# Kernel tuning notes

Measured on AMD Instinct MI355X. Metric: run time of the kernel, lower is better.

The kernel has to match this reference:

```python
import jax, jax.numpy as jnp
import numpy as np

NEIGH = 0.4  # neighborhood_size from the module


def setup_inputs() -> dict:
    key = jax.random.key(0)
    ks = jax.random.split(key, 14)
    N, E, H, G, M = 1024, 64, 128, 8, 20
    OUT = 6 * M
    f32 = jnp.float32
    inp = {
        "xabs": jax.random.uniform(ks[0], (N, 2), f32),
        "i_h0": jax.random.normal(ks[1], (1, N, H), f32) * 0.1,
        "i_c0": jax.random.normal(ks[2], (1, N, H), f32) * 0.1,
        # I_Embedding: Linear(2, E)
        "W_emb": jax.random.normal(ks[3], (E, 2), f32) * 0.5,
        "b_emb": jax.random.normal(ks[4], (E,), f32) * 0.1,
        # embedding_social: Linear(G*G*H, E)
        "W_soc": jax.random.normal(ks[5], (E, G * G * H), f32) * (1.0 / np.sqrt(G * G * H)),
        "b_soc": jax.random.normal(ks[6], (E,), f32) * 0.1,
        # LSTM(2E -> H), torch gate order [i, f, g, o]
        "W_ih": jax.random.normal(ks[7], (4 * H, 2 * E), f32) * (1.0 / np.sqrt(2 * E)),
        "W_hh": jax.random.normal(ks[8], (4 * H, H), f32) * (1.0 / np.sqrt(H)),
        "b_ih": jax.random.normal(ks[9], (4 * H,), f32) * 0.05,
        "b_hh": jax.random.normal(ks[10], (4 * H,), f32) * 0.05,
        # I_Output: Linear(H, 6*M)
        "W_out": jax.random.normal(ks[11], (OUT, H), f32) * (1.0 / np.sqrt(H)),
        "b_out": jax.random.normal(ks[12], (OUT,), f32) * 0.05,
    }
    return inp


def _grid_mask(xabs, G):
    # Vectorized getGridMask: [N, N, G*G] one-hot bin membership.
    N = xabs.shape[0]
    # dx[n, m] = other_x - width_low(n); in-range iff 0 <= dx < NEIGH
    dx = xabs[None, :, 0] - (xabs[:, None, 0] - NEIGH / 2)
    dy = xabs[None, :, 1] - (xabs[:, None, 1] - NEIGH / 2)
    cell_x = jnp.floor(dx / NEIGH * G).astype(jnp.int32)
    cell_y = jnp.floor(dy / NEIGH * G).astype(jnp.int32)
    valid = (dx >= 0) & (dx < NEIGH) & (dy >= 0) & (dy < NEIGH)
    valid &= (cell_x >= 0) & (cell_x < G) & (cell_y >= 0) & (cell_y < G)
    valid &= ~jnp.eye(N, dtype=bool)  # skip self
    cell = jnp.where(valid, cell_x + cell_y * G, 0)
    mask = jax.nn.one_hot(cell, G * G, dtype=xabs.dtype)
    return mask * valid[:, :, None].astype(xabs.dtype)


def reference(xabs, i_h0, i_c0, W_emb, b_emb, W_soc, b_soc,
              W_ih, W_hh, b_ih, b_hh, W_out, b_out):
    N = xabs.shape[0]
    H = i_h0.shape[-1]
    G = int(np.sqrt(W_soc.shape[1] // H))
    M = W_out.shape[0] // 6

    # Input embedding
    emb_x = jax.nn.relu(xabs @ W_emb.T + b_emb)  # [N, E]

    # Social pooling: grid mask + scatter-reduce of hidden states
    h0 = i_h0[0]  # [N, H]
    mask = _grid_mask(xabs, G)  # [N, N, G*G]
    social = jnp.einsum('nmg,md->ngd', mask, h0)  # [N, G*G, H]
    social = social.reshape(N, G * G * H)
    pooling = jax.nn.relu(social @ W_soc.T + b_soc)  # [N, E]

    # Single LSTM step (seq len 1, 1 layer), torch gate order i,f,g,o
    lstm_in = jnp.concatenate([emb_x, pooling], axis=-1)  # [N, 2E]
    gates = lstm_in @ W_ih.T + b_ih + h0 @ W_hh.T + b_hh  # [N, 4H]
    i_g, f_g, g_g, o_g = jnp.split(gates, 4, axis=-1)
    c = jax.nn.sigmoid(f_g) * i_c0[0] + jax.nn.sigmoid(i_g) * jnp.tanh(g_g)
    h = jax.nn.sigmoid(o_g) * jnp.tanh(c)  # [N, H]

    final = h @ W_out.T + b_out  # [N, 6M]
    mu1, mu2, log_sigma1, log_sigma2, rho, pi_logits = jnp.split(final, 6, axis=1)
    return (mu1, mu2, log_sigma1, log_sigma2, rho, pi_logits)
```

## Files before the change

kernel.cpp:

```cpp
#include <hip/hip_runtime.h>
#include <hip/hip_bf16.h>
#include <math.h>

typedef __hip_bfloat16 bf16;
typedef short s8v __attribute__((ext_vector_type(8)));
typedef float f4v __attribute__((ext_vector_type(4)));

__device__ __forceinline__ float b2f(bf16 v) { return __bfloat162float(v); }

template <bool F32>
__device__ __forceinline__ float ld(const void* p, int i) {
  if (F32) return ((const float*)p)[i];
  return b2f(((const bf16*)p)[i]);
}

template <bool F32>
__device__ __forceinline__ s8v ldfrag(const void* p, size_t i) {
  if (F32) {
    const float* f = (const float*)p + i;
    float4 u = *reinterpret_cast<const float4*>(f);
    float4 v = *reinterpret_cast<const float4*>(f + 4);
    s8v r;
    bf16 t;
    t = __float2bfloat16(u.x); r[0] = *(short*)&t;
    t = __float2bfloat16(u.y); r[1] = *(short*)&t;
    t = __float2bfloat16(u.z); r[2] = *(short*)&t;
    t = __float2bfloat16(u.w); r[3] = *(short*)&t;
    t = __float2bfloat16(v.x); r[4] = *(short*)&t;
    t = __float2bfloat16(v.y); r[5] = *(short*)&t;
    t = __float2bfloat16(v.z); r[6] = *(short*)&t;
    t = __float2bfloat16(v.w); r[7] = *(short*)&t;
    return r;
  }
  return *reinterpret_cast<const s8v*>((const bf16*)p + i);
}

__device__ __forceinline__ float sigm(float x) {
  return 0.5f * (1.0f + tanhf(0.5f * x));
}

__device__ __forceinline__ bool detect_f32(const void* xabs) {
  unsigned short v = ((const unsigned short*)xabs)[threadIdx.x & 63];
  int ex = (v >> 7) & 0xFF;
  return __ballot(ex >= 0x93) != 0ull;
}

template <bool F32>
__device__ __forceinline__ void cvt4(const void* src, bf16* __restrict__ dst,
                                     int count, int gt, int gsz) {
  for (int i = gt * 4; i < count; i += gsz * 4) {
    if (F32) {
      float4 v = *reinterpret_cast<const float4*>((const float*)src + i);
      bf16 t[4] = {__float2bfloat16(v.x), __float2bfloat16(v.y),
                   __float2bfloat16(v.z), __float2bfloat16(v.w)};
      *reinterpret_cast<uint2*>(&dst[i]) = *reinterpret_cast<uint2*>(t);
    } else {
      *reinterpret_cast<uint2*>(&dst[i]) =
          *reinterpret_cast<const uint2*>((const bf16*)src + i);
    }
  }
}

template <bool F32>
__device__ __forceinline__ void zgemm_body(const void* h0, const void* Wsoc,
                                           const void* Wih, const void* Whh,
                                           const void* Wout,
                                           bf16* __restrict__ Z, bf16* Wih_b,
                                           bf16* Whh_b, bf16* Wout_b) {
  if (blockIdx.x >= 256) {
    const int gt = (blockIdx.x - 256) * 256 + threadIdx.x;
    const int gsz = 16 * 256;
    cvt4<F32>(Wih, Wih_b, 512 * 128, gt, gsz);
    cvt4<F32>(Whh, Whh_b, 512 * 128, gt, gsz);
    cvt4<F32>(Wout, Wout_b, 120 * 128, gt, gsz);
    return;
  }
  const int wave = threadIdx.x >> 6, lane = threadIdx.x & 63;
  const int mt = blockIdx.x & 15;
  const int g  = (blockIdx.x >> 4) * 4 + wave;
  const int r16 = lane & 15, quad = lane >> 4;

  s8v afr[4][4];
#pragma unroll
  for (int ms = 0; ms < 4; ++ms)
#pragma unroll
    for (int kq = 0; kq < 4; ++kq)
      afr[ms][kq] = ldfrag<F32>(
          h0, (size_t)(mt * 64 + ms * 16 + r16) * 128 + kq * 32 + quad * 8);

  f4v acc[4][4];
#pragma unroll
  for (int ms = 0; ms < 4; ++ms)
#pragma unroll
    for (int t = 0; t < 4; ++t) acc[ms][t] = (f4v){0.f, 0.f, 0.f, 0.f};

#pragma unroll
  for (int t = 0; t < 4; ++t) {
#pragma unroll
    for (int kq = 0; kq < 4; ++kq) {
      s8v bfr = ldfrag<F32>(
          Wsoc, (size_t)(t * 16 + r16) * 8192 + g * 128 + kq * 32 + quad * 8);
#pragma unroll
      for (int ms = 0; ms < 4; ++ms)
        acc[ms][t] = __builtin_amdgcn_mfma_f32_16x16x32_bf16(afr[ms][kq], bfr,
                                                             acc[ms][t], 0, 0, 0);
    }
  }
#pragma unroll
  for (int ms = 0; ms < 4; ++ms)
#pragma unroll
    for (int t = 0; t < 4; ++t)
#pragma unroll
      for (int reg = 0; reg < 4; ++reg)
        Z[(size_t)(mt * 64 + ms * 16 + quad * 4 + reg) * 4096 + g * 64 +
          t * 16 + r16] = __float2bfloat16(acc[ms][t][reg]);
}

__global__ __launch_bounds__(256, 1) void k_zgemm(
    const void* h0, const void* Wsoc, const void* Wih, const void* Whh,
    const void* Wout, bf16* __restrict__ Z, bf16* Wih_b, bf16* Whh_b,
    bf16* Wout_b, const void* xabs) {
  if (detect_f32(xabs))
    zgemm_body<true>(h0, Wsoc, Wih, Whh, Wout, Z, Wih_b, Whh_b, Wout_b);
  else
    zgemm_body<false>(h0, Wsoc, Wih, Whh, Wout, Z, Wih_b, Whh_b, Wout_b);
}

#define XS 264
#define HS 136

template <bool F32>
__device__ __forceinline__ void fused_body(
    const void* xabs, const void* h0, const void* Wemb, const void* bemb,
    const void* bsoc, const bf16* __restrict__ Wih_b,
    const bf16* __restrict__ Whh_b, const void* bih, const void* bhh,
    const void* c0, const bf16* __restrict__ Wout_b, const void* bout,
    const bf16* __restrict__ Z, void* out, char* smem) {
  float* G   = (float*)smem;
  int* lists = (int*)smem;
  bf16* Xb   = (bf16*)(smem + 32768);
  bf16* Hb   = (bf16*)(smem + 32768 + 16 * XS * 2);
  const int tid = threadIdx.x;
  const int wave = tid >> 6, lane = tid & 63;
  const int r16 = lane & 15, quad = lane >> 4;

  for (int idx = 4 * XS + tid; idx < 16 * XS; idx += 256)
    Xb[idx] = __float2bfloat16(0.f);
  for (int idx = 4 * HS + tid; idx < 16 * HS; idx += 256)
    Hb[idx] = __float2bfloat16(0.f);

  const int n = blockIdx.x * 4 + wave;
  const float xn = ld<F32>(xabs, 2 * n);
  const float yn = ld<F32>(xabs, 2 * n + 1);
  const float tx = xn - 0.2f, ty = yn - 0.2f;
  int* mylist = lists + wave * 1024;
  int cnt = 0;
  for (int c = 0; c < 16; ++c) {
    const int m = c * 64 + lane;
    float dx = ld<F32>(xabs, 2 * m) - tx;
    float dy = ld<F32>(xabs, 2 * m + 1) - ty;
    int cx = (int)floorf(dx / 0.4f * 8.0f);
    int cy = (int)floorf(dy / 0.4f * 8.0f);
    bool valid = (dx >= 0.f) & (dx < 0.4f) & (dy >= 0.f) & (dy < 0.4f) &
                 (cx >= 0) & (cx < 8) & (cy >= 0) & (cy < 8) & (m != n);
    unsigned long long msk = __ballot(valid);
    if (valid) {
      int pos = cnt + __popcll(msk & ((1ull << lane) - 1ull));
      mylist[pos] = (m << 6) | (cx + cy * 8);
    }
    cnt += __popcll(msk);
  }
  float a0 = 0.f, a1 = 0.f, a2 = 0.f, a3 = 0.f;
  float a4 = 0.f, a5 = 0.f, a6 = 0.f, a7 = 0.f;
  int i = 0;
  for (; i + 8 <= cnt; i += 8) {
    int e0 = mylist[i],     e1 = mylist[i + 1];
    int e2 = mylist[i + 2], e3 = mylist[i + 3];
    int e4 = mylist[i + 4], e5 = mylist[i + 5];
    int e6 = mylist[i + 6], e7 = mylist[i + 7];
    a0 += b2f(Z[(size_t)(e0 >> 6) * 4096 + (e0 & 63) * 64 + lane]);
    a1 += b2f(Z[(size_t)(e1 >> 6) * 4096 + (e1 & 63) * 64 + lane]);
    a2 += b2f(Z[(size_t)(e2 >> 6) * 4096 + (e2 & 63) * 64 + lane]);
    a3 += b2f(Z[(size_t)(e3 >> 6) * 4096 + (e3 & 63) * 64 + lane]);
    a4 += b2f(Z[(size_t)(e4 >> 6) * 4096 + (e4 & 63) * 64 + lane]);
    a5 += b2f(Z[(size_t)(e5 >> 6) * 4096 + (e5 & 63) * 64 + lane]);
    a6 += b2f(Z[(size_t)(e6 >> 6) * 4096 + (e6 & 63) * 64 + lane]);
    a7 += b2f(Z[(size_t)(e7 >> 6) * 4096 + (e7 & 63) * 64 + lane]);
  }
  for (; i < cnt; ++i) {
    int e0 = mylist[i];
    a0 += b2f(Z[(size_t)(e0 >> 6) * 4096 + (e0 & 63) * 64 + lane]);
  }
  float pool = ((a0 + a1) + (a2 + a3)) + ((a4 + a5) + (a6 + a7));
  pool = fmaxf(pool + ld<F32>(bsoc, lane), 0.f);
  float emb = fmaxf(ld<F32>(Wemb, lane * 2) * xn +
                        ld<F32>(Wemb, lane * 2 + 1) * yn + ld<F32>(bemb, lane),
                    0.f);
  Xb[wave * XS + lane] = __float2bfloat16(emb);
  Xb[wave * XS + 64 + lane] = __float2bfloat16(pool);
  Xb[wave * XS + 128 + lane] = __float2bfloat16(ld<F32>(h0, n * 128 + lane));
  Xb[wave * XS + 192 + lane] =
      __float2bfloat16(ld<F32>(h0, n * 128 + 64 + lane));
  __syncthreads();

  s8v afr[8];
#pragma unroll
  for (int kq = 0; kq < 8; ++kq)
    afr[kq] = *reinterpret_cast<const s8v*>(&Xb[r16 * XS + kq * 32 + quad * 8]);
  const int j0w = wave * 128;
  f4v bacc[8];
#pragma unroll
  for (int jt = 0; jt < 8; ++jt) bacc[jt] = (f4v){0.f, 0.f, 0.f, 0.f};
#pragma unroll
  for (int jt = 0; jt < 8; ++jt) {
    int j = j0w + jt * 16 + r16;
#pragma unroll
    for (int kq = 0; kq < 4; ++kq) {
      s8v bfr = *reinterpret_cast<const s8v*>(
          &Wih_b[(size_t)j * 128 + kq * 32 + quad * 8]);
      bacc[jt] = __builtin_amdgcn_mfma_f32_16x16x32_bf16(afr[kq], bfr, bacc[jt],
                                                         0, 0, 0);
    }
#pragma unroll
    for (int kq = 0; kq < 4; ++kq) {
      s8v bfr = *reinterpret_cast<const s8v*>(
          &Whh_b[(size_t)j * 128 + kq * 32 + quad * 8]);
      bacc[jt] = __builtin_amdgcn_mfma_f32_16x16x32_bf16(afr[kq + 4], bfr,
                                                         bacc[jt], 0, 0, 0);
    }
  }
#pragma unroll
  for (int jt = 0; jt < 8; ++jt) {
    int j = j0w + jt * 16 + r16;
    float bias = ld<F32>(bih, j) + ld<F32>(bhh, j);
#pragma unroll
    for (int reg = 0; reg < 4; ++reg)
      G[(quad * 4 + reg) * 512 + j] = bacc[jt][reg] + bias;
  }
  __syncthreads();

  for (int idx = tid; idx < 512; idx += 256) {
    int m = idx >> 7, tt = idx & 127;
    float ig = G[m * 512 + tt], fg = G[m * 512 + 128 + tt];
    float gg = G[m * 512 + 256 + tt], og = G[m * 512 + 384 + tt];
    float c = sigm(fg) * ld<F32>(c0, (blockIdx.x * 4 + m) * 128 + tt) +
              sigm(ig) * tanhf(gg);
    Hb[m * HS + tt] = __float2bfloat16(sigm(og) * tanhf(c));
  }
  __syncthreads();

  s8v hfr[4];
#pragma unroll
  for (int kq = 0; kq < 4; ++kq)
    hfr[kq] = *reinterpret_cast<const s8v*>(&Hb[r16 * HS + kq * 32 + quad * 8]);
#pragma unroll
  for (int jt2 = 0; jt2 < 2; ++jt2) {
    int j = wave * 32 + jt2 * 16 + r16;
    int jj = j < 120 ? j : 119;
    f4v oacc = (f4v){0.f, 0.f, 0.f, 0.f};
#pragma unroll
    for (int kq = 0; kq < 4; ++kq) {
      s8v bfr = *reinterpret_cast<const s8v*>(
          &Wout_b[(size_t)jj * 128 + kq * 32 + quad * 8]);
      oacc = __builtin_amdgcn_mfma_f32_16x16x32_bf16(hfr[kq], bfr, oacc, 0, 0, 0);
    }
    if (j < 120 && quad == 0) {
      float bo = ld<F32>(bout, j);
      int kk = j / 20, mm = j % 20;
#pragma unroll
      for (int reg = 0; reg < 4; ++reg) {
        int oi = kk * 20480 + (blockIdx.x * 4 + reg) * 20 + mm;
        float val = oacc[reg] + bo;
        if (F32) ((float*)out)[oi] = val;
        else     ((bf16*)out)[oi] = __float2bfloat16(val);
      }
    }
  }
}

__global__ __launch_bounds__(256, 1) void k_fused(
    const void* xabs, const void* h0, const void* Wemb, const void* bemb,
    const void* bsoc, const bf16* Wih_b, const bf16* Whh_b, const void* bih,
    const void* bhh, const void* c0, const bf16* Wout_b, const void* bout,
    const bf16* __restrict__ Z, void* out) {
  __shared__ __align__(16) char smem[32768 + 16 * XS * 2 + 16 * HS * 2];
  if (detect_f32(xabs))
    fused_body<true>(xabs, h0, Wemb, bemb, bsoc, Wih_b, Whh_b, bih, bhh, c0,
                     Wout_b, bout, Z, out, smem);
  else
    fused_body<false>(xabs, h0, Wemb, bemb, bsoc, Wih_b, Whh_b, bih, bhh, c0,
                      Wout_b, bout, Z, out, smem);
}

extern "C" void kernel_launch(void* const* d_in, const int* in_sizes, int n_in,
                              void* d_out, int out_size, void* d_ws, size_t ws_size,
                              hipStream_t stream) {
  const void* xabs = d_in[0];
  const void* h0   = d_in[1];
  const void* c0   = d_in[2];
  const void* Wemb = d_in[3];
  const void* bemb = d_in[4];
  const void* Wsoc = d_in[5];
  const void* bsoc = d_in[6];
  const void* Wih  = d_in[7];
  const void* Whh  = d_in[8];
  const void* bih  = d_in[9];
  const void* bhh  = d_in[10];
  const void* Wout = d_in[11];
  const void* bout = d_in[12];

  bf16* Z      = (bf16*)d_ws;
  bf16* Wih_b  = Z + (size_t)1024 * 4096;
  bf16* Whh_b  = Wih_b + (size_t)512 * 128;
  bf16* Wout_b = Whh_b + (size_t)512 * 128;

  k_zgemm<<<dim3(272), dim3(256), 0, stream>>>(h0, Wsoc, Wih, Whh, Wout, Z,
                                               Wih_b, Whh_b, Wout_b, xabs);
  k_fused<<<dim3(256), dim3(256), 0, stream>>>(xabs, h0, Wemb, bemb, bsoc,
                                               Wih_b, Whh_b, bih, bhh, c0,
                                               Wout_b, bout, Z, d_out);
}
```

Before: 124.3 us.

## Merge Z-GEMM and fused LSTM kernels into one cooperative launch with grid sync

Replaces the two back-to-back kernel launches with a single cooperative kernel of 256 blocks. The blocks first do the weight conversion and the Z GEMM, then pass a grid-wide barrier, then run the fused embedding/pooling/LSTM/output phase. The weight conversion that used to run in 16 extra blocks is now spread across all blocks ahead of their GEMM tiles. This removes one launch and the inter-kernel gap, but adds grid-sync overhead and requires every block to be co-resident.

```diff
diff --git a/kernel.cpp b/kernel.cpp
--- a/kernel.cpp
+++ b/kernel.cpp
@@ -1,6 +1,9 @@
 #include <hip/hip_runtime.h>
 #include <hip/hip_bf16.h>
+#include <hip/hip_cooperative_groups.h>
 #include <math.h>
+
+namespace cg = cooperative_groups;
 
 typedef __hip_bfloat16 bf16;
 typedef short s8v __attribute__((ext_vector_type(8)));
@@ -62,19 +65,16 @@
 }
 
 template <bool F32>
-__device__ __forceinline__ void zgemm_body(const void* h0, const void* Wsoc,
-                                           const void* Wih, const void* Whh,
-                                           const void* Wout,
-                                           bf16* __restrict__ Z, bf16* Wih_b,
-                                           bf16* Whh_b, bf16* Wout_b) {
-  if (blockIdx.x >= 256) {
-    const int gt = (blockIdx.x - 256) * 256 + threadIdx.x;
-    const int gsz = 16 * 256;
-    cvt4<F32>(Wih, Wih_b, 512 * 128, gt, gsz);
-    cvt4<F32>(Whh, Whh_b, 512 * 128, gt, gsz);
-    cvt4<F32>(Wout, Wout_b, 120 * 128, gt, gsz);
-    return;
-  }
+__device__ __forceinline__ void phaseA(const void* h0, const void* Wsoc,
+                                       const void* Wih, const void* Whh,
+                                       const void* Wout, bf16* __restrict__ Z,
+                                       bf16* Wih_b, bf16* Whh_b, bf16* Wout_b) {
+  const int gt = blockIdx.x * 256 + threadIdx.x;
+  const int gsz = 256 * 256;
+  cvt4<F32>(Wih, Wih_b, 512 * 128, gt, gsz);
+  cvt4<F32>(Whh, Whh_b, 512 * 128, gt, gsz);
+  cvt4<F32>(Wout, Wout_b, 120 * 128, gt, gsz);
+
   const int wave = threadIdx.x >> 6, lane = threadIdx.x & 63;
   const int mt = blockIdx.x & 15;
   const int g  = (blockIdx.x >> 4) * 4 + wave;
@@ -116,21 +116,11 @@
           t * 16 + r16] = __float2bfloat16(acc[ms][t][reg]);
 }
 
-__global__ __launch_bounds__(256, 1) void k_zgemm(
-    const void* h0, const void* Wsoc, const void* Wih, const void* Whh,
-    const void* Wout, bf16* __restrict__ Z, bf16* Wih_b, bf16* Whh_b,
-    bf16* Wout_b, const void* xabs) {
-  if (detect_f32(xabs))
-    zgemm_body<true>(h0, Wsoc, Wih, Whh, Wout, Z, Wih_b, Whh_b, Wout_b);
-  else
-    zgemm_body<false>(h0, Wsoc, Wih, Whh, Wout, Z, Wih_b, Whh_b, Wout_b);
-}
-
 #define XS 264
 #define HS 136
 
 template <bool F32>
-__device__ __forceinline__ void fused_body(
+__device__ __forceinline__ void phaseB(
     const void* xabs, const void* h0, const void* Wemb, const void* bemb,
     const void* bsoc, const bf16* __restrict__ Wih_b,
     const bf16* __restrict__ Whh_b, const void* bih, const void* bhh,
@@ -278,18 +268,26 @@
   }
 }
 
-__global__ __launch_bounds__(256, 1) void k_fused(
-    const void* xabs, const void* h0, const void* Wemb, const void* bemb,
-    const void* bsoc, const bf16* Wih_b, const bf16* Whh_b, const void* bih,
-    const void* bhh, const void* c0, const bf16* Wout_b, const void* bout,
-    const bf16* __restrict__ Z, void* out) {
+__global__ __launch_bounds__(256, 1) void k_all(
+    const void* xabs, const void* h0, const void* c0, const void* Wemb,
+    const void* bemb, const void* Wsoc, const void* bsoc, const void* Wih,
+    const void* Whh, const void* bih, const void* bhh, const void* Wout,
+    const void* bout, bf16* __restrict__ Z, bf16* Wih_b, bf16* Whh_b,
+    bf16* Wout_b, void* out) {
   __shared__ __align__(16) char smem[32768 + 16 * XS * 2 + 16 * HS * 2];
-  if (detect_f32(xabs))
-    fused_body<true>(xabs, h0, Wemb, bemb, bsoc, Wih_b, Whh_b, bih, bhh, c0,
-                     Wout_b, bout, Z, out, smem);
+  const bool f32 = detect_f32(xabs);
+  if (f32) phaseA<true>(h0, Wsoc, Wih, Whh, Wout, Z, Wih_b, Whh_b, Wout_b);
+  else     phaseA<false>(h0, Wsoc, Wih, Whh, Wout, Z, Wih_b, Whh_b, Wout_b);
+
+  __threadfence();
+  cg::this_grid().sync();
+
+  if (f32)
+    phaseB<true>(xabs, h0, Wemb, bemb, bsoc, Wih_b, Whh_b, bih, bhh, c0,
+                 Wout_b, bout, Z, out, smem);
   else
-    fused_body<false>(xabs, h0, Wemb, bemb, bsoc, Wih_b, Whh_b, bih, bhh, c0,
-                      Wout_b, bout, Z, out, smem);
+    phaseB<false>(xabs, h0, Wemb, bemb, bsoc, Wih_b, Whh_b, bih, bhh, c0,
+                  Wout_b, bout, Z, out, smem);
 }
 
 extern "C" void kernel_launch(void* const* d_in, const int* in_sizes, int n_in,
@@ -308,15 +306,15 @@
   const void* bhh  = d_in[10];
   const void* Wout = d_in[11];
   const void* bout = d_in[12];
+  void* outp = d_out;
 
   bf16* Z      = (bf16*)d_ws;
   bf16* Wih_b  = Z + (size_t)1024 * 4096;
   bf16* Whh_b  = Wih_b + (size_t)512 * 128;
   bf16* Wout_b = Whh_b + (size_t)512 * 128;
 
-  k_zgemm<<<dim3(272), dim3(256), 0, stream>>>(h0, Wsoc, Wih, Whh, Wout, Z,
-                                               Wih_b, Whh_b, Wout_b, xabs);
-  k_fused<<<dim3(256), dim3(256), 0, stream>>>(xabs, h0, Wemb, bemb, bsoc,
-                                               Wih_b, Whh_b, bih, bhh, c0,
-                                               Wout_b, bout, Z, d_out);
-}
+  void* args[] = {&xabs, &h0, &c0, &Wemb, &bemb, &Wsoc, &bsoc, &Wih, &Whh,
+                  &bih, &bhh, &Wout, &bout, &Z, &Wih_b, &Whh_b, &Wout_b, &outp};
+  hipLaunchCooperativeKernel((void*)k_all, dim3(256), dim3(256), args, 0,
+                             stream);
+}
```

New measurement: 224.0 us. 80.2% more time.
